# Kernel tuning notes

Hardware: AMD Instinct MI355X
Metric: run time of the kernel (lower is better)

The kernel has to match this reference:

```python
import jax, jax.numpy as jnp
import numpy as np

N = 50000      # nodes
E = 800000     # edges (avg degree 16)
IN = 128       # input feature dim
HID = 32       # per-head hidden dim
OUT = 64       # per-head output dim
H = 2          # heads per layer
NEG = 0.2      # leaky relu negative slope


def setup_inputs() -> dict:
    key = jax.random.key(0)
    ks = jax.random.split(key, 16)
    x = jax.random.normal(ks[0], (N, IN), dtype=jnp.float32)
    src = jax.random.randint(ks[1], (E,), 0, N)
    dst = jax.random.randint(ks[2], (E,), 0, N)

    def lin(k, fin, fout):
        return jax.random.normal(k, (fin, fout), dtype=jnp.float32) * (1.0 / np.sqrt(fin))

    def attn(k, h, d):
        return jax.random.normal(k, (h, d), dtype=jnp.float32) * 0.1

    # layer 0: IN -> H*HID, layer 1: H*HID -> H*HID, layer 2 (output): H*HID -> H*OUT
    W0, al0, ar0, b0 = lin(ks[3], IN, H * HID), attn(ks[4], H, HID), attn(ks[5], H, HID), jnp.zeros((H * HID,), jnp.float32)
    W1, al1, ar1, b1 = lin(ks[6], H * HID, H * HID), attn(ks[7], H, HID), attn(ks[8], H, HID), jnp.zeros((H * HID,), jnp.float32)
    W2, al2, ar2, b2 = lin(ks[9], H * HID, H * OUT), attn(ks[10], H, OUT), attn(ks[11], H, OUT), jnp.zeros((H * OUT,), jnp.float32)
    return {"x": x, "src": src, "dst": dst,
            "W0": W0, "al0": al0, "ar0": ar0, "b0": b0,
            "W1": W1, "al1": al1, "ar1": ar1, "b1": b1,
            "W2": W2, "al2": al2, "ar2": ar2, "b2": b2}


def gat_conv(x, src, dst, W, al, ar, b, heads, out_dim, apply_relu):
    # feat: [N, H, D]
    feat = (x @ W).reshape(-1, heads, out_dim)
    el = jnp.einsum('nhd,hd->nh', feat, al)   # [N, H]
    er = jnp.einsum('nhd,hd->nh', feat, ar)   # [N, H]
    # per-edge attention logits, leaky-relu
    e = jax.nn.leaky_relu(el[src] + er[dst], NEG)          # [E, H]
    # edge softmax over incoming edges of each dst node (numerically stable)
    m = jax.ops.segment_max(e, dst, num_segments=N)        # [N, H]
    m = jnp.where(jnp.isfinite(m), m, 0.0)                 # nodes w/o in-edges
    ex = jnp.exp(e - m[dst])                               # [E, H]
    s = jax.ops.segment_sum(ex, dst, num_segments=N)       # [N, H]
    alpha = ex / s[dst]                                    # [E, H]
    # weighted aggregate of source features into dst nodes
    rst = jax.ops.segment_sum(feat[src] * alpha[:, :, None], dst, num_segments=N)  # [N, H, D]
    rst = rst + b.reshape(1, heads, out_dim)
    if apply_relu:
        rst = jax.nn.relu(rst)
    return rst


def reference(x, src, dst, W0, al0, ar0, b0, W1, al1, ar1, b1, W2, al2, ar2, b2):
    h = gat_conv(x, src, dst, W0, al0, ar0, b0, H, HID, True).reshape(N, H * HID)   # flatten(1)
    h = gat_conv(h, src, dst, W1, al1, ar1, b1, H, HID, True).reshape(N, H * HID)   # flatten(1)
    logits = gat_conv(h, src, dst, W2, al2, ar2, b2, H, OUT, False).mean(axis=1)    # mean over heads -> [N, OUT]
    return logits
```

## Files before the change

### kernel.cpp

```cpp
#include <hip/hip_runtime.h>
#include <hip/hip_bf16.h>
#include <hip/hip_fp16.h>

#define NNODES 50000
#define NEG_SLOPE 0.2f
#define BKT_SHIFT 8
#define NBKT ((NNODES + 255) >> 8)
#define STRIDE 5120
#define PCHUNK 2048
#define PEPT 8

typedef _Float16 half8 __attribute__((ext_vector_type(8)));
typedef float v4f __attribute__((ext_vector_type(4)));

__device__ __forceinline__ int rfl(int v) { return __builtin_amdgcn_readfirstlane(v); }

__device__ __forceinline__ void pack_one(const float* W, _Float16* Wp, int K, int C, int tid) {
    int KC = K / 32;
    int l = tid & 63;
    int kc = (tid >> 6) % KC;
    int t = tid / (KC * 64);
    int cc = l & 15, q = l >> 4;
    half8 b;
#pragma unroll
    for (int j = 0; j < 8; j++)
        b[j] = (_Float16)W[(size_t)(kc * 32 + q * 8 + j) * C + t * 16 + cc];
    *(half8*)(Wp + (size_t)tid * 8) = b;
}

__global__ __launch_bounds__(256) void kernelAB(
    const float* __restrict__ x, const float* __restrict__ W0,
    const float* __restrict__ AL, const float* __restrict__ AR,
    _Float16* __restrict__ featA, float2* __restrict__ el2A, float2* __restrict__ er2A,
    const float* __restrict__ W2, _Float16* __restrict__ Wp2,
    const int* __restrict__ src, const int* __restrict__ dst,
    int* __restrict__ bcursor, int2* __restrict__ ebuf, int E, int N) {
    int blk = blockIdx.x;
    if (blk >= 786) {
        __shared__ int hist[NBKT];
        __shared__ int gbase[NBKT];
        int t = threadIdx.x;
        for (int i = t; i < NBKT; i += 256) hist[i] = 0;
        __syncthreads();
        int base = (blk - 786) * PCHUNK;
        int sreg[PEPT], dreg[PEPT], rreg[PEPT], breg[PEPT];
#pragma unroll
        for (int k = 0; k < PEPT; k++) {
            int i = base + k * 256 + t;
            if (i < E) {
                sreg[k] = src[i];
                dreg[k] = dst[i];
                breg[k] = dreg[k] >> BKT_SHIFT;
                rreg[k] = atomicAdd(&hist[breg[k]], 1);
            } else {
                breg[k] = -1;
            }
        }
        __syncthreads();
        for (int i = t; i < NBKT; i += 256)
            if (hist[i]) gbase[i] = i * STRIDE + atomicAdd(&bcursor[i * 16], hist[i]);
        __syncthreads();
#pragma unroll
        for (int k = 0; k < PEPT; k++) {
            if (breg[k] >= 0)
                ebuf[(size_t)(gbase[breg[k]] + rreg[k])] = make_int2(sreg[k], dreg[k]);
        }
        return;
    }
    if (blk >= 782) {
        int tid = (blk - 782) * 256 + threadIdx.x;
        if (tid < 8 * 2 * 64) pack_one(W2, Wp2, 64, 128, tid);
        return;
    }
    int wave = threadIdx.x >> 6, lane = threadIdx.x & 63;
    int mtile = blk * 4 + wave;
    if (mtile * 16 >= N) return;
    int m0 = mtile * 16;
    int c = lane & 15, q = lane >> 4;
    v4f acc[4];
#pragma unroll
    for (int t = 0; t < 4; t++) acc[t] = (v4f){0.f, 0.f, 0.f, 0.f};
    const size_t arow = (size_t)(m0 + c) * 128 + q * 8;
#pragma unroll
    for (int kc = 0; kc < 4; kc++) {
        const float* xr = x + arow + kc * 32;
        float4 f0 = *(const float4*)xr;
        float4 f1 = *(const float4*)(xr + 4);
        float fv[8] = {f0.x, f0.y, f0.z, f0.w, f1.x, f1.y, f1.z, f1.w};
        half8 ah, av;
#pragma unroll
        for (int j = 0; j < 8; j++) {
            ah[j] = (_Float16)fv[j];
            av[j] = (_Float16)(fv[j] - (float)ah[j]);
        }
#pragma unroll
        for (int tt = 0; tt < 4; tt++) {
            half8 b;
#pragma unroll
            for (int j = 0; j < 8; j++)
                b[j] = (_Float16)W0[(size_t)(kc * 32 + q * 8 + j) * 64 + tt * 16 + c];
            acc[tt] = __builtin_amdgcn_mfma_f32_16x16x32_f16(ah, b, acc[tt], 0, 0, 0);
            acc[tt] = __builtin_amdgcn_mfma_f32_16x16x32_f16(av, b, acc[tt], 0, 0, 0);
        }
    }
#pragma unroll
    for (int tt = 0; tt < 4; tt++)
#pragma unroll
        for (int r = 0; r < 4; r++) {
            int row = m0 + q * 4 + r;
            featA[(size_t)row * 64 + tt * 16 + c] = (_Float16)acc[tt][r];
        }
    float alv[4], arv[4];
#pragma unroll
    for (int tt = 0; tt < 4; tt++) { alv[tt] = AL[tt * 16 + c]; arv[tt] = AR[tt * 16 + c]; }
#pragma unroll
    for (int r = 0; r < 4; r++) {
        float l0 = 0.f, l1 = 0.f, r0 = 0.f, r1 = 0.f;
#pragma unroll
        for (int tt = 0; tt < 4; tt++) {
            float v = acc[tt][r];
            if (tt < 2) { l0 = fmaf(v, alv[tt], l0); r0 = fmaf(v, arv[tt], r0); }
            else        { l1 = fmaf(v, alv[tt], l1); r1 = fmaf(v, arv[tt], r1); }
        }
#pragma unroll
        for (int m = 1; m < 16; m <<= 1) {
            l0 += __shfl_xor(l0, m, 64);
            l1 += __shfl_xor(l1, m, 64);
            r0 += __shfl_xor(r0, m, 64);
            r1 += __shfl_xor(r1, m, 64);
        }
        if (c == 0) {
            int row = m0 + q * 4 + r;
            el2A[row] = make_float2(l0, l1);
            er2A[row] = make_float2(r0, r1);
        }
    }
}

__global__ __launch_bounds__(256) void local_sort(const int2* __restrict__ ebuf,
                                                  const int* __restrict__ bcursor,
                                                  int2* __restrict__ rowse,
                                                  int* __restrict__ csrc, int N) {
    __shared__ int lcnt[256], lrow[256], ws[4];
    int b = blockIdx.x;
    int d0 = b << BKT_SHIFT;
    int t = threadIdx.x;
    int base = b * STRIDE;
    int endE = base + bcursor[b * 16];
    lcnt[t] = 0;
    __syncthreads();
    for (int i = base + t; i < endE; i += 256)
        atomicAdd(&lcnt[ebuf[i].y - d0], 1);
    __syncthreads();
    int v = lcnt[t];
    int lane = t & 63;
    int x = v;
#pragma unroll
    for (int m = 1; m < 64; m <<= 1) {
        int y = __shfl_up(x, m, 64);
        if (lane >= m) x += y;
    }
    if (lane == 63) ws[t >> 6] = x;
    __syncthreads();
    int w = t >> 6, waveoff = 0;
#pragma unroll
    for (int k = 0; k < 4; k++) if (k < w) waveoff += ws[k];
    int excl = base + waveoff + x - v;
    lrow[t] = excl;
    int d = d0 + t;
    if (d < N) rowse[d] = make_int2(excl, excl + v);
    lcnt[t] = 0;
    __syncthreads();
    for (int i = base + t; i < endE; i += 256) {
        int2 e = ebuf[i];
        int ld = e.y - d0;
        int p = lrow[ld] + atomicAdd(&lcnt[ld], 1);
        csrc[p] = e.x;
    }
}

__global__ __launch_bounds__(256) void agg0_gemm1(
    const int2* __restrict__ rowse, const int* __restrict__ csrc,
    const float2* __restrict__ el2A, const float2* __restrict__ er2A,
    const _Float16* __restrict__ featA, const float* __restrict__ b0,
    const float* __restrict__ W1, const float* __restrict__ al1, const float* __restrict__ ar1,
    _Float16* __restrict__ featB, float2* __restrict__ el2B, float2* __restrict__ er2B,
    int N) {
    __shared__ int2 stA[4][64], stB[4][64];
    __shared__ float vbuf[4][64];
    __shared__ float4 w1v[16 * 64];
    int wave = threadIdx.x >> 6, lane = threadIdx.x & 63, h = lane >> 5;
    for (int i = threadIdx.x; i < 64 * 64; i += 256) {
        int k = i >> 6, cc = i & 63;
        ((float*)w1v)[((((k >> 2) << 6) + cc) << 2) | (k & 3)] = W1[i];
    }
    __syncthreads();
    float bl = b0[lane];
    float al1v = al1[lane], ar1v = ar1[lane];
    const int2* stH = h ? stB[wave] : stA[wave];
    for (int n0 = blockIdx.x * 4 + wave; n0 < N; n0 += gridDim.x * 4) {
        int n = rfl(n0);
        int2 se = rowse[n];
        int beg = rfl(se.x), end = rfl(se.y);
        float2 rr = er2A[n];
        float s = 0.f, acc = 0.f;
        for (int base = beg; base < end; base += 64) {
            int idx = base + lane;
            int sv = 0; float wxv = 0.f, wyv = 0.f;
            if (idx < end) {
                sv = csrc[idx];
                float2 l = el2A[sv];
                float t0 = l.x + rr.x; t0 = t0 > 0.f ? t0 : NEG_SLOPE * t0;
                float t1 = l.y + rr.y; t1 = t1 > 0.f ? t1 : NEG_SLOPE * t1;
                wxv = __expf(t0); wyv = __expf(t1);
            }
            stA[wave][lane] = make_int2(sv, __float_as_int(wxv));
            stB[wave][lane] = make_int2(sv, __float_as_int(wyv));
            int cnt = (min(64, end - base) + 7) & ~7;
            for (int j = 0; j < cnt; j += 8) {
                int4 e01 = *(const int4*)(stH + j);
                int4 e23 = *(const int4*)(stH + j + 2);
                int4 e45 = *(const int4*)(stH + j + 4);
                int4 e67 = *(const int4*)(stH + j + 6);
                float f0 = (float)featA[(size_t)e01.x * 64 + lane];
                float f1 = (float)featA[(size_t)e01.z * 64 + lane];
                float f2 = (float)featA[(size_t)e23.x * 64 + lane];
                float f3 = (float)featA[(size_t)e23.z * 64 + lane];
                float f4 = (float)featA[(size_t)e45.x * 64 + lane];
                float f5 = (float)featA[(size_t)e45.z * 64 + lane];
                float f6 = (float)featA[(size_t)e67.x * 64 + lane];
                float f7 = (float)featA[(size_t)e67.z * 64 + lane];
                float w0 = __int_as_float(e01.y), w1 = __int_as_float(e01.w);
                float w2 = __int_as_float(e23.y), w3 = __int_as_float(e23.w);
                float w4 = __int_as_float(e45.y), w5 = __int_as_float(e45.w);
                float w6 = __int_as_float(e67.y), w7 = __int_as_float(e67.w);
                s += ((w0 + w1) + (w2 + w3)) + ((w4 + w5) + (w6 + w7));
                acc = fmaf(w0, f0, acc);
                acc = fmaf(w1, f1, acc);
                acc = fmaf(w2, f2, acc);
                acc = fmaf(w3, f3, acc);
                acc = fmaf(w4, f4, acc);
                acc = fmaf(w5, f5, acc);
                acc = fmaf(w6, f6, acc);
                acc = fmaf(w7, f7, acc);
            }
        }
        float v = (s > 0.f) ? acc / s : 0.f;
        v = fmaxf(v + bl, 0.f);
        vbuf[wave][lane] = v;
        const float4* vv = (const float4*)vbuf[wave];
        float f = 0.f;
#pragma unroll
        for (int kk = 0; kk < 16; kk++) {
            float4 v4 = vv[kk];
            float4 w4 = w1v[(kk << 6) + lane];
            f = fmaf(v4.x, w4.x, f);
            f = fmaf(v4.y, w4.y, f);
            f = fmaf(v4.z, w4.z, f);
            f = fmaf(v4.w, w4.w, f);
        }
        featB[(size_t)n * 64 + lane] = (_Float16)f;
        float vl = f * al1v, vr = f * ar1v;
#pragma unroll
        for (int m = 1; m < 32; m <<= 1) {
            vl += __shfl_xor(vl, m, 64);
            vr += __shfl_xor(vr, m, 64);
        }
        if ((lane & 31) == 0) {
            ((float*)el2B)[n * 2 + h] = vl;
            ((float*)er2B)[n * 2 + h] = vr;
        }
    }
}

__global__ __launch_bounds__(256) void aggregate32(
    const int2* __restrict__ rowse, const int* __restrict__ csrc,
    const float2* __restrict__ el2, const float2* __restrict__ er2,
    const _Float16* __restrict__ feat16, const float* __restrict__ b,
    _Float16* __restrict__ ahi, _Float16* __restrict__ alo, int N) {
    __shared__ int2 stA[4][64], stB[4][64];
    int wave = threadIdx.x >> 6, lane = threadIdx.x & 63, h = lane >> 5;
    int n = rfl(blockIdx.x * 4 + wave);
    if (n >= N) return;
    float bl = b[lane];
    int2 se = rowse[n];
    int beg = rfl(se.x), end = rfl(se.y);
    float2 rr = er2[n];
    const int2* stH = h ? stB[wave] : stA[wave];
    float s = 0.f, acc = 0.f;
    for (int base = beg; base < end; base += 64) {
        int idx = base + lane;
        int sv = 0; float wxv = 0.f, wyv = 0.f;
        if (idx < end) {
            sv = csrc[idx];
            float2 l = el2[sv];
            float t0 = l.x + rr.x; t0 = t0 > 0.f ? t0 : NEG_SLOPE * t0;
            float t1 = l.y + rr.y; t1 = t1 > 0.f ? t1 : NEG_SLOPE * t1;
            wxv = __expf(t0); wyv = __expf(t1);
        }
        stA[wave][lane] = make_int2(sv, __float_as_int(wxv));
        stB[wave][lane] = make_int2(sv, __float_as_int(wyv));
        int cnt = (min(64, end - base) + 7) & ~7;
        for (int j = 0; j < cnt; j += 8) {
            int4 e01 = *(const int4*)(stH + j);
            int4 e23 = *(const int4*)(stH + j + 2);
            int4 e45 = *(const int4*)(stH + j + 4);
            int4 e67 = *(const int4*)(stH + j + 6);
            float f0 = (float)feat16[(size_t)e01.x * 64 + lane];
            float f1 = (float)feat16[(size_t)e01.z * 64 + lane];
            float f2 = (float)feat16[(size_t)e23.x * 64 + lane];
            float f3 = (float)feat16[(size_t)e23.z * 64 + lane];
            float f4 = (float)feat16[(size_t)e45.x * 64 + lane];
            float f5 = (float)feat16[(size_t)e45.z * 64 + lane];
            float f6 = (float)feat16[(size_t)e67.x * 64 + lane];
            float f7 = (float)feat16[(size_t)e67.z * 64 + lane];
            float w0 = __int_as_float(e01.y), w1 = __int_as_float(e01.w);
            float w2 = __int_as_float(e23.y), w3 = __int_as_float(e23.w);
            float w4 = __int_as_float(e45.y), w5 = __int_as_float(e45.w);
            float w6 = __int_as_float(e67.y), w7 = __int_as_float(e67.w);
            s += ((w0 + w1) + (w2 + w3)) + ((w4 + w5) + (w6 + w7));
            acc = fmaf(w0, f0, acc);
            acc = fmaf(w1, f1, acc);
            acc = fmaf(w2, f2, acc);
            acc = fmaf(w3, f3, acc);
            acc = fmaf(w4, f4, acc);
            acc = fmaf(w5, f5, acc);
            acc = fmaf(w6, f6, acc);
            acc = fmaf(w7, f7, acc);
        }
    }
    float v = (s > 0.f) ? acc / s : 0.f;
    v = fmaxf(v + bl, 0.f);
    _Float16 hv = (_Float16)v;
    ahi[(size_t)n * 64 + lane] = hv;
    alo[(size_t)n * 64 + lane] = (_Float16)(v - (float)hv);
}

__global__ __launch_bounds__(256) void gemm_mfma2(
    const _Float16* __restrict__ Ahi, const _Float16* __restrict__ Alo,
    const _Float16* __restrict__ Wp,
    const float* __restrict__ AL, const float* __restrict__ AR,
    __half2* __restrict__ feat2, float2* __restrict__ el2, float2* __restrict__ er2,
    int N) {
    constexpr int KC = 2, NT = 8;
    int wave = threadIdx.x >> 6, lane = threadIdx.x & 63;
    int mtile = blockIdx.x * 4 + wave;
    if (mtile * 16 >= N) return;
    int m0 = mtile * 16;
    int c = lane & 15, q = lane >> 4;
    v4f acc[NT];
#pragma unroll
    for (int t = 0; t < NT; t++) acc[t] = (v4f){0.f, 0.f, 0.f, 0.f};
    const size_t arow = (size_t)(m0 + c) * 64 + q * 8;
#pragma unroll
    for (int kc = 0; kc < KC; kc++) {
        half8 ah = *(const half8*)(Ahi + arow + kc * 32);
        half8 av = *(const half8*)(Alo + arow + kc * 32);
#pragma unroll
        for (int t = 0; t < NT; t++) {
            half8 b = *(const half8*)(Wp + ((size_t)(t * KC + kc) * 64 + lane) * 8);
            acc[t] = __builtin_amdgcn_mfma_f32_16x16x32_f16(ah, b, acc[t], 0, 0, 0);
            acc[t] = __builtin_amdgcn_mfma_f32_16x16x32_f16(av, b, acc[t], 0, 0, 0);
        }
    }
#pragma unroll
    for (int t = 0; t < NT / 2; t++)
#pragma unroll
        for (int r = 0; r < 4; r++) {
            int row = m0 + q * 4 + r;
            feat2[(size_t)row * 64 + t * 16 + c] =
                __floats2half2_rn(acc[t][r], acc[t + NT / 2][r]);
        }
    float alv[NT], arv[NT];
#pragma unroll
    for (int t = 0; t < NT; t++) { alv[t] = AL[t * 16 + c]; arv[t] = AR[t * 16 + c]; }
#pragma unroll
    for (int r = 0; r < 4; r++) {
        float l0 = 0.f, l1 = 0.f, r0 = 0.f, r1 = 0.f;
#pragma unroll
        for (int t = 0; t < NT; t++) {
            float v = acc[t][r];
            if (t < NT / 2) { l0 = fmaf(v, alv[t], l0); r0 = fmaf(v, arv[t], r0); }
            else            { l1 = fmaf(v, alv[t], l1); r1 = fmaf(v, arv[t], r1); }
        }
#pragma unroll
        for (int m = 1; m < 16; m <<= 1) {
            l0 += __shfl_xor(l0, m, 64);
            l1 += __shfl_xor(l1, m, 64);
            r0 += __shfl_xor(r0, m, 64);
            r1 += __shfl_xor(r1, m, 64);
        }
        if (c == 0) {
            int row = m0 + q * 4 + r;
            el2[row] = make_float2(l0, l1);
            er2[row] = make_float2(r0, r1);
        }
    }
}

__global__ __launch_bounds__(256) void aggregate64_mean(
    const int2* __restrict__ rowse, const int* __restrict__ csrc,
    const float2* __restrict__ el2, const float2* __restrict__ er2,
    const __half2* __restrict__ feat2, const float* __restrict__ b,
    float* __restrict__ out, int N) {
    __shared__ int4 st[4][64];
    int wave = threadIdx.x >> 6, lane = threadIdx.x & 63;
    int n = rfl(blockIdx.x * 4 + wave);
    if (n >= N) return;
    float b0 = b[lane], b1 = b[64 + lane];
    int2 se = rowse[n];
    int beg = rfl(se.x), end = rfl(se.y);
    float2 rr = er2[n];
    float s0 = 0.f, s1 = 0.f, a0 = 0.f, a1 = 0.f;
    for (int base = beg; base < end; base += 64) {
        int idx = base + lane;
        int sv = 0; float wxv = 0.f, wyv = 0.f;
        if (idx < end) {
            sv = csrc[idx];
            float2 l = el2[sv];
            float t0 = l.x + rr.x; t0 = t0 > 0.f ? t0 : NEG_SLOPE * t0;
            float t1 = l.y + rr.y; t1 = t1 > 0.f ? t1 : NEG_SLOPE * t1;
            wxv = __expf(t0); wyv = __expf(t1);
        }
        st[wave][lane] = make_int4(sv, __float_as_int(wxv), __float_as_int(wyv), 0);
        int cnt = (min(64, end - base) + 7) & ~7;
        for (int j = 0; j < cnt; j += 8) {
            float2 fv[8]; float wxs[8], wys[8];
#pragma unroll
            for (int u = 0; u < 8; u++) {
                int4 e = st[wave][j + u];
                wxs[u] = __int_as_float(e.y);
                wys[u] = __int_as_float(e.z);
                fv[u] = __half22float2(feat2[(size_t)e.x * 64 + lane]);
            }
#pragma unroll
            for (int u = 0; u < 8; u++) {
                s0 += wxs[u]; s1 += wys[u];
                a0 = fmaf(wxs[u], fv[u].x, a0);
                a1 = fmaf(wys[u], fv[u].y, a1);
            }
        }
    }
    float v0 = (s0 > 0.f) ? a0 / s0 : 0.f;
    float v1 = (s1 > 0.f) ? a1 / s1 : 0.f;
    out[(size_t)n * 64 + lane] = 0.5f * ((v0 + b0) + (v1 + b1));
}


extern "C" void kernel_launch(void* const* d_in, const int* in_sizes, int n_in,
                              void* d_out, int out_size, void* d_ws, size_t ws_size,
                              hipStream_t stream) {
    const float* x   = (const float*)d_in[0];
    const int*   src = (const int*)d_in[1];
    const int*   dst = (const int*)d_in[2];
    const float* W0  = (const float*)d_in[3];
    const float* al0 = (const float*)d_in[4];
    const float* ar0 = (const float*)d_in[5];
    const float* b0  = (const float*)d_in[6];
    const float* W1  = (const float*)d_in[7];
    const float* al1 = (const float*)d_in[8];
    const float* ar1 = (const float*)d_in[9];
    const float* b1  = (const float*)d_in[10];
    const float* W2  = (const float*)d_in[11];
    const float* al2 = (const float*)d_in[12];
    const float* ar2 = (const float*)d_in[13];
    const float* b2  = (const float*)d_in[14];
    float* out = (float*)d_out;

    const int N = NNODES;
    const int E = in_sizes[1];

    char* p = (char*)d_ws;
    auto alloc = [&](size_t bytes) {
        void* r = (void*)p;
        p += (bytes + 255) & ~(size_t)255;
        return r;
    };
    int*    bcursor = (int*)alloc((size_t)NBKT * 16 * 4);
    int2*   rowse   = (int2*)alloc((size_t)N * 8);
    int2*   ebuf    = (int2*)alloc(((size_t)NBKT * STRIDE + 4096) * 8);
    int*    csrc    = (int*)alloc(((size_t)NBKT * STRIDE + 4096) * 4);
    float2* el2A    = (float2*)alloc((size_t)N * 8);
    float2* er2A    = (float2*)alloc((size_t)N * 8);
    float2* el2B    = (float2*)alloc((size_t)N * 8);
    float2* er2B    = (float2*)alloc((size_t)N * 8);
    _Float16* ahi   = (_Float16*)alloc((size_t)N * 64 * 2);
    _Float16* alo   = (_Float16*)alloc((size_t)N * 64 * 2);
    void*   featA   = alloc((size_t)N * 64 * 4);
    _Float16* featB = (_Float16*)alloc((size_t)N * 64 * 2);
    _Float16* Wp2   = (_Float16*)alloc(8 * 2 * 64 * 8 * 2);

    hipMemsetAsync(bcursor, 0, (size_t)NBKT * 16 * 4, stream);
    int nch = (E + PCHUNK - 1) / PCHUNK;
    kernelAB<<<786 + nch, 256, 0, stream>>>(x, W0, al0, ar0, (_Float16*)featA, el2A, er2A,
                                            W2, Wp2, src, dst, bcursor, ebuf, E, N);
    local_sort<<<NBKT, 256, 0, stream>>>(ebuf, bcursor, rowse, csrc, N);

    int nb4 = (N + 3) / 4;
    agg0_gemm1<<<2048, 256, 0, stream>>>(rowse, csrc, el2A, er2A, (const _Float16*)featA,
                                         b0, W1, al1, ar1, featB, el2B, er2B, N);
    aggregate32<<<nb4, 256, 0, stream>>>(rowse, csrc, el2B, er2B, featB, b1, ahi, alo, N);
    int gb = (N / 16 + 3) / 4;
    gemm_mfma2<<<gb, 256, 0, stream>>>(ahi, alo, Wp2, al2, ar2, (__half2*)featA, el2A, er2A, N);
    aggregate64_mean<<<nb4, 256, 0, stream>>>(rowse, csrc, el2A, er2A, (const __half2*)featA,
                                              b2, out, N);
}
```

Baseline: 226.9 us.

## Fuse layer-1 aggregation into layer-2 MFMA GEMM; widen sort blocks and unroll gathers

Merges the layer-1 aggregation kernel with the layer-2 MFMA GEMM. Each wave aggregates 16 destination nodes into an LDS tile, then splits the values into hi/lo fp16 on the fly, which removes the ahi/alo round trip through global memory and one launch. It also grows local_sort to 1024 threads per block and unrolls the edge gather loops from 8 to 16 edges per step to keep more loads in flight. The risks are lower parallelism in the fused kernel (one wave serially handles 16 nodes, only about 780 blocks), more register pressure from the wider unroll, and extra wasted padded edges on low-degree nodes.

```diff
diff --git a/kernel.cpp b/kernel.cpp
--- a/kernel.cpp
+++ b/kernel.cpp
@@ -137,22 +137,22 @@
     }
 }
 
-__global__ __launch_bounds__(256) void local_sort(const int2* __restrict__ ebuf,
-                                                  const int* __restrict__ bcursor,
-                                                  int2* __restrict__ rowse,
-                                                  int* __restrict__ csrc, int N) {
+__global__ __launch_bounds__(1024) void local_sort(const int2* __restrict__ ebuf,
+                                                   const int* __restrict__ bcursor,
+                                                   int2* __restrict__ rowse,
+                                                   int* __restrict__ csrc, int N) {
     __shared__ int lcnt[256], lrow[256], ws[4];
     int b = blockIdx.x;
     int d0 = b << BKT_SHIFT;
     int t = threadIdx.x;
     int base = b * STRIDE;
     int endE = base + bcursor[b * 16];
-    lcnt[t] = 0;
+    if (t < 256) lcnt[t] = 0;
     __syncthreads();
-    for (int i = base + t; i < endE; i += 256)
+    for (int i = base + t; i < endE; i += 1024)
         atomicAdd(&lcnt[ebuf[i].y - d0], 1);
     __syncthreads();
-    int v = lcnt[t];
+    int v = (t < 256) ? lcnt[t] : 0;
     int lane = t & 63;
     int x = v;
 #pragma unroll
@@ -160,18 +160,20 @@
         int y = __shfl_up(x, m, 64);
         if (lane >= m) x += y;
     }
-    if (lane == 63) ws[t >> 6] = x;
+    if (t < 256 && lane == 63) ws[t >> 6] = x;
     __syncthreads();
-    int w = t >> 6, waveoff = 0;
-#pragma unroll
-    for (int k = 0; k < 4; k++) if (k < w) waveoff += ws[k];
-    int excl = base + waveoff + x - v;
-    lrow[t] = excl;
-    int d = d0 + t;
-    if (d < N) rowse[d] = make_int2(excl, excl + v);
-    lcnt[t] = 0;
+    if (t < 256) {
+        int w = t >> 6, waveoff = 0;
+#pragma unroll
+        for (int k = 0; k < 4; k++) if (k < w) waveoff += ws[k];
+        int excl = base + waveoff + x - v;
+        lrow[t] = excl;
+        int d = d0 + t;
+        if (d < N) rowse[d] = make_int2(excl, excl + v);
+        lcnt[t] = 0;
+    }
     __syncthreads();
-    for (int i = base + t; i < endE; i += 256) {
+    for (int i = base + t; i < endE; i += 1024) {
         int2 e = ebuf[i];
         int ld = e.y - d0;
         int p = lrow[ld] + atomicAdd(&lcnt[ld], 1);
@@ -216,33 +218,21 @@
             }
             stA[wave][lane] = make_int2(sv, __float_as_int(wxv));
             stB[wave][lane] = make_int2(sv, __float_as_int(wyv));
-            int cnt = (min(64, end - base) + 7) & ~7;
-            for (int j = 0; j < cnt; j += 8) {
-                int4 e01 = *(const int4*)(stH + j);
-                int4 e23 = *(const int4*)(stH + j + 2);
-                int4 e45 = *(const int4*)(stH + j + 4);
-                int4 e67 = *(const int4*)(stH + j + 6);
-                float f0 = (float)featA[(size_t)e01.x * 64 + lane];
-                float f1 = (float)featA[(size_t)e01.z * 64 + lane];
-                float f2 = (float)featA[(size_t)e23.x * 64 + lane];
-                float f3 = (float)featA[(size_t)e23.z * 64 + lane];
-                float f4 = (float)featA[(size_t)e45.x * 64 + lane];
-                float f5 = (float)featA[(size_t)e45.z * 64 + lane];
-                float f6 = (float)featA[(size_t)e67.x * 64 + lane];
-                float f7 = (float)featA[(size_t)e67.z * 64 + lane];
-                float w0 = __int_as_float(e01.y), w1 = __int_as_float(e01.w);
-                float w2 = __int_as_float(e23.y), w3 = __int_as_float(e23.w);
-                float w4 = __int_as_float(e45.y), w5 = __int_as_float(e45.w);
-                float w6 = __int_as_float(e67.y), w7 = __int_as_float(e67.w);
-                s += ((w0 + w1) + (w2 + w3)) + ((w4 + w5) + (w6 + w7));
-                acc = fmaf(w0, f0, acc);
-                acc = fmaf(w1, f1, acc);
-                acc = fmaf(w2, f2, acc);
-                acc = fmaf(w3, f3, acc);
-                acc = fmaf(w4, f4, acc);
-                acc = fmaf(w5, f5, acc);
-                acc = fmaf(w6, f6, acc);
-                acc = fmaf(w7, f7, acc);
+            int cnt = (min(64, end - base) + 15) & ~15;
+            for (int j = 0; j < cnt; j += 16) {
+                float f[16], w[16];
+#pragma unroll
+                for (int u = 0; u < 16; u += 2) {
+                    int4 e = *(const int4*)(stH + j + u);
+                    w[u]     = __int_as_float(e.y);
+                    w[u + 1] = __int_as_float(e.w);
+                    f[u]     = (float)featA[(size_t)e.x * 64 + lane];
+                    f[u + 1] = (float)featA[(size_t)e.z * 64 + lane];
+                }
+                s += ((w[0] + w[1]) + (w[2] + w[3])) + ((w[4] + w[5]) + (w[6] + w[7]));
+                s += ((w[8] + w[9]) + (w[10] + w[11])) + ((w[12] + w[13]) + (w[14] + w[15]));
+#pragma unroll
+                for (int u = 0; u < 16; u++) acc = fmaf(w[u], f[u], acc);
             }
         }
         float v = (s > 0.f) ? acc / s : 0.f;
@@ -273,115 +263,102 @@
     }
 }
 
-__global__ __launch_bounds__(256) void aggregate32(
+__global__ __launch_bounds__(256) void agg1_gemm2(
     const int2* __restrict__ rowse, const int* __restrict__ csrc,
     const float2* __restrict__ el2, const float2* __restrict__ er2,
     const _Float16* __restrict__ feat16, const float* __restrict__ b,
-    _Float16* __restrict__ ahi, _Float16* __restrict__ alo, int N) {
-    __shared__ int2 stA[4][64], stB[4][64];
-    int wave = threadIdx.x >> 6, lane = threadIdx.x & 63, h = lane >> 5;
-    int n = rfl(blockIdx.x * 4 + wave);
-    if (n >= N) return;
-    float bl = b[lane];
-    int2 se = rowse[n];
-    int beg = rfl(se.x), end = rfl(se.y);
-    float2 rr = er2[n];
-    const int2* stH = h ? stB[wave] : stA[wave];
-    float s = 0.f, acc = 0.f;
-    for (int base = beg; base < end; base += 64) {
-        int idx = base + lane;
-        int sv = 0; float wxv = 0.f, wyv = 0.f;
-        if (idx < end) {
-            sv = csrc[idx];
-            float2 l = el2[sv];
-            float t0 = l.x + rr.x; t0 = t0 > 0.f ? t0 : NEG_SLOPE * t0;
-            float t1 = l.y + rr.y; t1 = t1 > 0.f ? t1 : NEG_SLOPE * t1;
-            wxv = __expf(t0); wyv = __expf(t1);
-        }
-        stA[wave][lane] = make_int2(sv, __float_as_int(wxv));
-        stB[wave][lane] = make_int2(sv, __float_as_int(wyv));
-        int cnt = (min(64, end - base) + 7) & ~7;
-        for (int j = 0; j < cnt; j += 8) {
-            int4 e01 = *(const int4*)(stH + j);
-            int4 e23 = *(const int4*)(stH + j + 2);
-            int4 e45 = *(const int4*)(stH + j + 4);
-            int4 e67 = *(const int4*)(stH + j + 6);
-            float f0 = (float)feat16[(size_t)e01.x * 64 + lane];
-            float f1 = (float)feat16[(size_t)e01.z * 64 + lane];
-            float f2 = (float)feat16[(size_t)e23.x * 64 + lane];
-            float f3 = (float)feat16[(size_t)e23.z * 64 + lane];
-            float f4 = (float)feat16[(size_t)e45.x * 64 + lane];
-            float f5 = (float)feat16[(size_t)e45.z * 64 + lane];
-            float f6 = (float)feat16[(size_t)e67.x * 64 + lane];
-            float f7 = (float)feat16[(size_t)e67.z * 64 + lane];
-            float w0 = __int_as_float(e01.y), w1 = __int_as_float(e01.w);
-            float w2 = __int_as_float(e23.y), w3 = __int_as_float(e23.w);
-            float w4 = __int_as_float(e45.y), w5 = __int_as_float(e45.w);
-            float w6 = __int_as_float(e67.y), w7 = __int_as_float(e67.w);
-            s += ((w0 + w1) + (w2 + w3)) + ((w4 + w5) + (w6 + w7));
-            acc = fmaf(w0, f0, acc);
-            acc = fmaf(w1, f1, acc);
-            acc = fmaf(w2, f2, acc);
-            acc = fmaf(w3, f3, acc);
-            acc = fmaf(w4, f4, acc);
-            acc = fmaf(w5, f5, acc);
-            acc = fmaf(w6, f6, acc);
-            acc = fmaf(w7, f7, acc);
-        }
-    }
-    float v = (s > 0.f) ? acc / s : 0.f;
-    v = fmaxf(v + bl, 0.f);
-    _Float16 hv = (_Float16)v;
-    ahi[(size_t)n * 64 + lane] = hv;
-    alo[(size_t)n * 64 + lane] = (_Float16)(v - (float)hv);
-}
-
-__global__ __launch_bounds__(256) void gemm_mfma2(
-    const _Float16* __restrict__ Ahi, const _Float16* __restrict__ Alo,
     const _Float16* __restrict__ Wp,
     const float* __restrict__ AL, const float* __restrict__ AR,
-    __half2* __restrict__ feat2, float2* __restrict__ el2, float2* __restrict__ er2,
+    __half2* __restrict__ feat2, float2* __restrict__ el2o, float2* __restrict__ er2o,
     int N) {
-    constexpr int KC = 2, NT = 8;
-    int wave = threadIdx.x >> 6, lane = threadIdx.x & 63;
+    __shared__ int2 stA[4][64], stB[4][64];
+    __shared__ float vt[4][64 * 17];
+    int wave = threadIdx.x >> 6, lane = threadIdx.x & 63, h = lane >> 5;
     int mtile = blockIdx.x * 4 + wave;
     if (mtile * 16 >= N) return;
     int m0 = mtile * 16;
+    float bl = b[lane];
+    const int2* stH = h ? stB[wave] : stA[wave];
+    float* vw = vt[wave];
+    for (int i = 0; i < 16; i++) {
+        int n = m0 + i;
+        int2 se = rowse[n];
+        int beg = rfl(se.x), end = rfl(se.y);
+        float2 rr = er2[n];
+        float s = 0.f, acc = 0.f;
+        for (int base = beg; base < end; base += 64) {
+            int idx = base + lane;
+            int sv = 0; float wxv = 0.f, wyv = 0.f;
+            if (idx < end) {
+                sv = csrc[idx];
+                float2 l = el2[sv];
+                float t0 = l.x + rr.x; t0 = t0 > 0.f ? t0 : NEG_SLOPE * t0;
+                float t1 = l.y + rr.y; t1 = t1 > 0.f ? t1 : NEG_SLOPE * t1;
+                wxv = __expf(t0); wyv = __expf(t1);
+            }
+            stA[wave][lane] = make_int2(sv, __float_as_int(wxv));
+            stB[wave][lane] = make_int2(sv, __float_as_int(wyv));
+            int cnt = (min(64, end - base) + 15) & ~15;
+            for (int j = 0; j < cnt; j += 16) {
+                float f[16], w[16];
+#pragma unroll
+                for (int u = 0; u < 16; u += 2) {
+                    int4 e = *(const int4*)(stH + j + u);
+                    w[u]     = __int_as_float(e.y);
+                    w[u + 1] = __int_as_float(e.w);
+                    f[u]     = (float)feat16[(size_t)e.x * 64 + lane];
+                    f[u + 1] = (float)feat16[(size_t)e.z * 64 + lane];
+                }
+                s += ((w[0] + w[1]) + (w[2] + w[3])) + ((w[4] + w[5]) + (w[6] + w[7]));
+                s += ((w[8] + w[9]) + (w[10] + w[11])) + ((w[12] + w[13]) + (w[14] + w[15]));
+#pragma unroll
+                for (int u = 0; u < 16; u++) acc = fmaf(w[u], f[u], acc);
+            }
+        }
+        float v = (s > 0.f) ? acc / s : 0.f;
+        v = fmaxf(v + bl, 0.f);
+        vw[lane * 17 + i] = v;
+    }
     int c = lane & 15, q = lane >> 4;
-    v4f acc[NT];
-#pragma unroll
-    for (int t = 0; t < NT; t++) acc[t] = (v4f){0.f, 0.f, 0.f, 0.f};
-    const size_t arow = (size_t)(m0 + c) * 64 + q * 8;
-#pragma unroll
-    for (int kc = 0; kc < KC; kc++) {
-        half8 ah = *(const half8*)(Ahi + arow + kc * 32);
-        half8 av = *(const half8*)(Alo + arow + kc * 32);
-#pragma unroll
-        for (int t = 0; t < NT; t++) {
-            half8 b = *(const half8*)(Wp + ((size_t)(t * KC + kc) * 64 + lane) * 8);
-            acc[t] = __builtin_amdgcn_mfma_f32_16x16x32_f16(ah, b, acc[t], 0, 0, 0);
-            acc[t] = __builtin_amdgcn_mfma_f32_16x16x32_f16(av, b, acc[t], 0, 0, 0);
-        }
-    }
-#pragma unroll
-    for (int t = 0; t < NT / 2; t++)
+    v4f acc2[8];
+#pragma unroll
+    for (int t = 0; t < 8; t++) acc2[t] = (v4f){0.f, 0.f, 0.f, 0.f};
+#pragma unroll
+    for (int kc = 0; kc < 2; kc++) {
+        half8 ah, av;
+#pragma unroll
+        for (int e = 0; e < 8; e++) {
+            float fv = vw[(kc * 32 + q * 8 + e) * 17 + c];
+            _Float16 hi = (_Float16)fv;
+            ah[e] = hi;
+            av[e] = (_Float16)(fv - (float)hi);
+        }
+#pragma unroll
+        for (int t = 0; t < 8; t++) {
+            half8 bf = *(const half8*)(Wp + ((size_t)(t * 2 + kc) * 64 + lane) * 8);
+            acc2[t] = __builtin_amdgcn_mfma_f32_16x16x32_f16(ah, bf, acc2[t], 0, 0, 0);
+            acc2[t] = __builtin_amdgcn_mfma_f32_16x16x32_f16(av, bf, acc2[t], 0, 0, 0);
+        }
+    }
+#pragma unroll
+    for (int t = 0; t < 4; t++)
 #pragma unroll
         for (int r = 0; r < 4; r++) {
             int row = m0 + q * 4 + r;
             feat2[(size_t)row * 64 + t * 16 + c] =
-                __floats2half2_rn(acc[t][r], acc[t + NT / 2][r]);
-        }
-    float alv[NT], arv[NT];
-#pragma unroll
-    for (int t = 0; t < NT; t++) { alv[t] = AL[t * 16 + c]; arv[t] = AR[t * 16 + c]; }
+                __floats2half2_rn(acc2[t][r], acc2[t + 4][r]);
+        }
+    float alv[8], arv[8];
+#pragma unroll
+    for (int t = 0; t < 8; t++) { alv[t] = AL[t * 16 + c]; arv[t] = AR[t * 16 + c]; }
 #pragma unroll
     for (int r = 0; r < 4; r++) {
         float l0 = 0.f, l1 = 0.f, r0 = 0.f, r1 = 0.f;
 #pragma unroll
-        for (int t = 0; t < NT; t++) {
-            float v = acc[t][r];
-            if (t < NT / 2) { l0 = fmaf(v, alv[t], l0); r0 = fmaf(v, arv[t], r0); }
-            else            { l1 = fmaf(v, alv[t], l1); r1 = fmaf(v, arv[t], r1); }
+        for (int t = 0; t < 8; t++) {
+            float v = acc2[t][r];
+            if (t < 4) { l0 = fmaf(v, alv[t], l0); r0 = fmaf(v, arv[t], r0); }
+            else       { l1 = fmaf(v, alv[t], l1); r1 = fmaf(v, arv[t], r1); }
         }
 #pragma unroll
         for (int m = 1; m < 16; m <<= 1) {
@@ -392,8 +369,8 @@
         }
         if (c == 0) {
             int row = m0 + q * 4 + r;
-            el2[row] = make_float2(l0, l1);
-            er2[row] = make_float2(r0, r1);
+            el2o[row] = make_float2(l0, l1);
+            er2o[row] = make_float2(r0, r1);
         }
     }
 }
@@ -423,18 +400,18 @@
             wxv = __expf(t0); wyv = __expf(t1);
         }
         st[wave][lane] = make_int4(sv, __float_as_int(wxv), __float_as_int(wyv), 0);
-        int cnt = (min(64, end - base) + 7) & ~7;
-        for (int j = 0; j < cnt; j += 8) {
-            float2 fv[8]; float wxs[8], wys[8];
-#pragma unroll
-            for (int u = 0; u < 8; u++) {
+        int cnt = (min(64, end - base) + 15) & ~15;
+        for (int j = 0; j < cnt; j += 16) {
+            float2 fv[16]; float wxs[16], wys[16];
+#pragma unroll
+            for (int u = 0; u < 16; u++) {
                 int4 e = st[wave][j + u];
                 wxs[u] = __int_as_float(e.y);
                 wys[u] = __int_as_float(e.z);
                 fv[u] = __half22float2(feat2[(size_t)e.x * 64 + lane]);
             }
 #pragma unroll
-            for (int u = 0; u < 8; u++) {
+            for (int u = 0; u < 16; u++) {
                 s0 += wxs[u]; s1 += wys[u];
                 a0 = fmaf(wxs[u], fv[u].x, a0);
                 a1 = fmaf(wys[u], fv[u].y, a1);
@@ -484,8 +461,6 @@
     float2* er2A    = (float2*)alloc((size_t)N * 8);
     float2* el2B    = (float2*)alloc((size_t)N * 8);
     float2* er2B    = (float2*)alloc((size_t)N * 8);
-    _Float16* ahi   = (_Float16*)alloc((size_t)N * 64 * 2);
-    _Float16* alo   = (_Float16*)alloc((size_t)N * 64 * 2);
     void*   featA   = alloc((size_t)N * 64 * 4);
     _Float16* featB = (_Float16*)alloc((size_t)N * 64 * 2);
     _Float16* Wp2   = (_Float16*)alloc(8 * 2 * 64 * 8 * 2);
@@ -494,14 +469,14 @@
     int nch = (E + PCHUNK - 1) / PCHUNK;
     kernelAB<<<786 + nch, 256, 0, stream>>>(x, W0, al0, ar0, (_Float16*)featA, el2A, er2A,
                                             W2, Wp2, src, dst, bcursor, ebuf, E, N);
-    local_sort<<<NBKT, 256, 0, stream>>>(ebuf, bcursor, rowse, csrc, N);
+    local_sort<<<NBKT, 1024, 0, stream>>>(ebuf, bcursor, rowse, csrc, N);
 
     int nb4 = (N + 3) / 4;
     agg0_gemm1<<<2048, 256, 0, stream>>>(rowse, csrc, el2A, er2A, (const _Float16*)featA,
                                          b0, W1, al1, ar1, featB, el2B, er2B, N);
-    aggregate32<<<nb4, 256, 0, stream>>>(rowse, csrc, el2B, er2B, featB, b1, ahi, alo, N);
-    int gb = (N / 16 + 3) / 4;
-    gemm_mfma2<<<gb, 256, 0, stream>>>(ahi, alo, Wp2, al2, ar2, (__half2*)featA, el2A, er2A, N);
+    int fb = (N / 16 + 3) / 4;
+    agg1_gemm2<<<fb, 256, 0, stream>>>(rowse, csrc, el2B, er2B, featB, b1, Wp2, al2, ar2,
+                                       (__half2*)featA, el2A, er2A, N);
     aggregate64_mean<<<nb4, 256, 0, stream>>>(rowse, csrc, el2A, er2A, (const __half2*)featA,
                                               b2, out, N);
 }
```

Measured after the change: 265.0 us. 16.8% more time.
